# Kernel optimization log

Measured on AMD Instinct MI355X. Metric: run time of the kernel, lower is better.

The kernel has to match this reference:

```python
import jax, jax.numpy as jnp
import numpy as np

E = 8        # num_experts
TOP_K = 2    # num_experts_per_tok
AUX_COEFF = 0.01


def _grok_ffn(x, g, u, d):
    # down(gelu(gate(x)) * up(x)); torch F.gelu default is exact (erf)
    return (jax.nn.gelu(x @ g.T, approximate=False) * (x @ u.T)) @ d.T


def setup_inputs() -> dict:
    key = jax.random.key(0)
    ks = jax.random.split(key, 8)
    B, T, D, H = 4, 4096, 1024, 2816
    s = 0.02
    return {
        "x": jax.random.normal(ks[0], (B, T, D), dtype=jnp.float32),
        "gate_w": jax.random.normal(ks[1], (E, D), dtype=jnp.float32) * 0.01,
        "wg": jax.random.normal(ks[2], (E, H, D), dtype=jnp.float32) * s,
        "wu": jax.random.normal(ks[3], (E, H, D), dtype=jnp.float32) * s,
        "wd": jax.random.normal(ks[4], (E, D, H), dtype=jnp.float32) * s,
        "sg": jax.random.normal(ks[5], (H, D), dtype=jnp.float32) * s,
        "su": jax.random.normal(ks[6], (H, D), dtype=jnp.float32) * s,
        "sd": jax.random.normal(ks[7], (D, H), dtype=jnp.float32) * s,
    }


def reference(x, gate_w, wg, wu, wd, sg, su, sd):
    B, T, D = x.shape
    xf = x.reshape(B * T, D)  # (N, D)

    # ---- router ----
    logits = (xf @ gate_w.T).astype(jnp.float32)          # (N, E)
    top_v, top_i = jax.lax.top_k(logits, TOP_K)           # (N, K)
    expert_weights = jax.nn.softmax(top_v, axis=-1)       # (N, K)
    gates = jax.nn.softmax(logits, axis=-1)               # (N, E)
    f = jax.nn.one_hot(top_i[:, 0], E, dtype=jnp.float32).mean(axis=0)
    P = gates.mean(axis=0)
    aux_loss = AUX_COEFF * E * (f * P).sum()

    # combine weight per (token, expert): sum_k w[t,k] * [idx[t,k]==e]
    onehot = jax.nn.one_hot(top_i, E, dtype=jnp.float32)  # (N, K, E)
    combine = (expert_weights[..., None] * onehot).sum(axis=1)  # (N, E)

    # ---- expert compute (loop over small fixed expert count) ----
    out = jnp.zeros_like(xf)
    for e in range(E):
        out = out + combine[:, e:e + 1] * _grok_ffn(xf, wg[e], wu[e], wd[e])

    out = out.reshape(B, T, D)
    out = out + _grok_ffn(x, sg, su, sd)  # shared expert
    return out, aux_loss
```

## Files before the change

### kernel.cpp

```cpp
#include <hip/hip_runtime.h>
#include <cstdint>

#define NE 8
#define NEX 9
#define NTOK 16384
#define DDIM 1024
#define HDIM 2816

typedef unsigned short u16;
typedef __attribute__((ext_vector_type(8))) short short8;
typedef __attribute__((ext_vector_type(4))) float f32x4;

__device__ __forceinline__ u16 f2bf(float f) {
  uint32_t u = __builtin_bit_cast(uint32_t, f);
  u += 0x7FFFu + ((u >> 16) & 1u);
  return (u16)(u >> 16);
}

__device__ __forceinline__ float wave_reduce_sum(float v) {
  for (int off = 32; off > 0; off >>= 1) v += __shfl_xor(v, off, 64);
  return v;
}

#define GLOAD16(gsrc, ldst)                                                   \
  __builtin_amdgcn_global_load_lds(                                           \
      (const __attribute__((address_space(1))) unsigned int*)(gsrc),          \
      (__attribute__((address_space(3))) unsigned int*)(ldst), 16, 0, 0)

__device__ __forceinline__ void xcd_map(int NT, int MT, int* nt, int* mt) {
  int lin = blockIdx.y * NT + blockIdx.x;
  int nwg = NT * MT;
  int q = nwg >> 3, r = nwg & 7;
  int xcd = lin & 7, idx = lin >> 3;
  int nl = (xcd < r) ? (xcd * (q + 1) + idx) : (r * (q + 1) + (xcd - r) * q + idx);
  *nt = nl / MT;
  *mt = nl % MT;
}

__global__ void init_kernel(int* cnt, float* Pacc, float* fcnt) {
  int t = threadIdx.x;
  if (t < NEX) cnt[t] = (t == 8) ? NTOK : 0;
  if (t < NE) { Pacc[t] = 0.f; fcnt[t] = 0.f; }
}

struct CvtArgs {
  const float* src[7];
  u16* dst[7];
  long long cum[8];
};

__global__ void convert_kernel(CvtArgs a) {
  long long stride = (long long)gridDim.x * blockDim.x;
  long long total = a.cum[7];
  for (long long g = (long long)blockIdx.x * blockDim.x + threadIdx.x; g < total; g += stride) {
    int s = 0;
    while (g >= a.cum[s + 1]) s++;
    long long off = (g - a.cum[s]) * 4;
    float4 v = *reinterpret_cast<const float4*>(a.src[s] + off);
    union { u16 u[4]; uint2 w; } o;
    o.u[0] = f2bf(v.x); o.u[1] = f2bf(v.y); o.u[2] = f2bf(v.z); o.u[3] = f2bf(v.w);
    *reinterpret_cast<uint2*>(a.dst[s] + off) = o.w;
  }
}

__global__ __launch_bounds__(256) void router_kernel(
    const float* __restrict__ x, const float* __restrict__ gw,
    int* __restrict__ tok, float* __restrict__ wtl,
    int* __restrict__ cnt, float* __restrict__ Pacc, float* __restrict__ fcnt,
    u16* __restrict__ xbf) {
  int lane = threadIdx.x & 63;
  int wv = threadIdx.x >> 6;
  __shared__ float red[4][16];
  float pP[NE], pF[NE];
#pragma unroll
  for (int e = 0; e < NE; e++) { pP[e] = 0.f; pF[e] = 0.f; }
  int t0 = blockIdx.x * 16 + wv * 4;
  for (int ti = 0; ti < 4; ti++) {
    int t = t0 + ti;
    float part[NE];
#pragma unroll
    for (int e = 0; e < NE; e++) part[e] = 0.f;
    const float* xp = x + (size_t)t * DDIM;
#pragma unroll
    for (int j = 0; j < 16; j++) {
      float xv = xp[lane + j * 64];
      xbf[(size_t)t * DDIM + lane + j * 64] = f2bf(xv);
#pragma unroll
      for (int e = 0; e < NE; e++) part[e] += xv * gw[e * DDIM + lane + j * 64];
    }
#pragma unroll
    for (int e = 0; e < NE; e++) part[e] = wave_reduce_sum(part[e]);
    if (lane == 0) {
      float v0 = -1e30f, v1 = -1e30f; int i0 = 0, i1 = 0;
#pragma unroll
      for (int e = 0; e < NE; e++) {
        float v = part[e];
        if (v > v0) { v1 = v0; i1 = i0; v0 = v; i0 = e; }
        else if (v > v1) { v1 = v; i1 = e; }
      }
      float e1 = expf(v1 - v0);
      float w0 = 1.f / (1.f + e1);
      float w1 = e1 * w0;
      float s = 0.f, g[NE];
#pragma unroll
      for (int e = 0; e < NE; e++) { g[e] = expf(part[e] - v0); s += g[e]; }
      float inv = 1.f / s;
#pragma unroll
      for (int e = 0; e < NE; e++) pP[e] += g[e] * inv;
      pF[i0] += 1.f;
      int p0 = atomicAdd(&cnt[i0], 1);
      tok[i0 * NTOK + p0] = t; wtl[i0 * NTOK + p0] = w0;
      int p1 = atomicAdd(&cnt[i1], 1);
      tok[i1 * NTOK + p1] = t; wtl[i1 * NTOK + p1] = w1;
      tok[8 * NTOK + t] = t; wtl[8 * NTOK + t] = 1.f;
    }
  }
  if (lane == 0) {
#pragma unroll
    for (int e = 0; e < NE; e++) { red[wv][e] = pP[e]; red[wv][e + 8] = pF[e]; }
  }
  __syncthreads();
  if (threadIdx.x < 16) {
    float s = red[0][threadIdx.x] + red[1][threadIdx.x] + red[2][threadIdx.x] + red[3][threadIdx.x];
    if (threadIdx.x < 8) atomicAdd(&Pacc[threadIdx.x], s);
    else atomicAdd(&fcnt[threadIdx.x - 8], s);
  }
}

__global__ void finalize_router(const int* cnt, int* offs, const float* Pacc,
                                const float* fcnt, float* out_aux) {
  if (threadIdx.x == 0 && blockIdx.x == 0) {
    int p = NTOK;
    for (int e = 0; e < NE; e++) { offs[e] = p; p += cnt[e]; }
    offs[8] = 0;
    float aux = 0.f;
    for (int e = 0; e < NE; e++)
      aux += (fcnt[e] * (1.f / NTOK)) * (Pacc[e] * (1.f / NTOK));
    *out_aux = 0.01f * 8.f * aux;
  }
}


template<bool WB>
__global__ __launch_bounds__(256, 2) void pass1_kernel(
    const u16* __restrict__ xbf, const void* __restrict__ WGall,
    const void* __restrict__ WUall, const void* __restrict__ SG,
    const void* __restrict__ SU, const int* __restrict__ tok,
    const int* __restrict__ cnt, const int* __restrict__ offs,
    u16* __restrict__ Abuf, int e0, int ab_off) {
  int nt, mt;
  xcd_map(gridDim.x, gridDim.y, &nt, &mt);
  int e = e0 + blockIdx.z;
  int Me = cnt[e];
  if (mt * 128 >= Me) return;
  int base = offs[e];
  int ab = (ab_off < 0) ? base : ab_off;

  __shared__ u16 lX[128 * 64];
  __shared__ u16 lG[128 * 64];
  __shared__ u16 lU[128 * 64];

  int tid = threadIdx.x, lane = tid & 63, wv = tid >> 6;
  int wr = wv >> 1, wc = wv & 1;
  size_t wst = (size_t)HDIM * DDIM;
  int swsrc = ((lane & 7) ^ (lane >> 3)) * 8;

  const u16* gx[4];
#pragma unroll
  for (int q = 0; q < 4; q++) {
    int r = (wv * 4 + q) * 8 + (lane >> 3);
    int gm = mt * 128 + r;
    int tk = (gm < Me) ? tok[e * NTOK + gm] : 0;
    gx[q] = xbf + (size_t)tk * DDIM + swsrc;
  }

  const u16 *gg[4], *gu[4];
  const float *pg0 = nullptr, *pu0 = nullptr;
  int st_r0 = 0, st_chunk = 0, st_win = 0;
  if constexpr (WB) {
    const u16* G = (e == 8) ? (const u16*)SG : (const u16*)WGall + (size_t)e * wst;
    const u16* U = (e == 8) ? (const u16*)SU : (const u16*)WUall + (size_t)e * wst;
#pragma unroll
    for (int q = 0; q < 4; q++) {
      int r = (wv * 4 + q) * 8 + (lane >> 3);
      gg[q] = G + (size_t)(nt * 128 + r) * DDIM + swsrc;
      gu[q] = U + (size_t)(nt * 128 + r) * DDIM + swsrc;
    }
  } else {
    const float* G = (e == 8) ? (const float*)SG : (const float*)WGall + (size_t)e * wst;
    const float* U = (e == 8) ? (const float*)SU : (const float*)WUall + (size_t)e * wst;
    st_r0 = wv * 32 + (lane >> 4);
    int c0 = (lane & 15) * 4;
    st_chunk = c0 >> 3; st_win = c0 & 7;
    pg0 = G + (size_t)(nt * 128 + st_r0) * DDIM + c0;
    pu0 = U + (size_t)(nt * 128 + st_r0) * DDIM + c0;
  }

  f32x4 accG[4][4] = {};
  f32x4 accU[4][4] = {};

  for (int kt = 0; kt < DDIM / 64; kt++) {
    __syncthreads();
    int ko = kt * 64;
#pragma unroll
    for (int q = 0; q < 4; q++)
      GLOAD16(gx[q] + ko, lX + (wv * 4 + q) * 512);
    if constexpr (WB) {
#pragma unroll
      for (int q = 0; q < 4; q++) {
        int ldsoff = (wv * 4 + q) * 512;
        GLOAD16(gg[q] + ko, lG + ldsoff);
        GLOAD16(gu[q] + ko, lU + ldsoff);
      }
    } else {
#pragma unroll
      for (int q = 0; q < 8; q++) {
        int row = st_r0 + q * 4;
        int pc = (((st_chunk ^ (row & 7)) << 3) | st_win);
        float4 vg = *reinterpret_cast<const float4*>(pg0 + ko + q * 4 * DDIM);
        float4 vu = *reinterpret_cast<const float4*>(pu0 + ko + q * 4 * DDIM);
        union { u16 h[4]; uint2 w; } og, ou;
        og.h[0] = f2bf(vg.x); og.h[1] = f2bf(vg.y); og.h[2] = f2bf(vg.z); og.h[3] = f2bf(vg.w);
        ou.h[0] = f2bf(vu.x); ou.h[1] = f2bf(vu.y); ou.h[2] = f2bf(vu.z); ou.h[3] = f2bf(vu.w);
        *reinterpret_cast<uint2*>(lG + row * 64 + pc) = og.w;
        *reinterpret_cast<uint2*>(lU + row * 64 + pc) = ou.w;
      }
    }
    asm volatile("s_waitcnt vmcnt(0)" ::: "memory");
    __syncthreads();

    __builtin_amdgcn_s_setprio(1);
#pragma unroll
    for (int kk = 0; kk < 2; kk++) {
      int kbs = (((kk * 4 + (lane >> 4)) ^ (lane & 7))) * 8;
      short8 af[4];
#pragma unroll
      for (int m = 0; m < 4; m++) {
        int row = wr * 64 + m * 16 + (lane & 15);
        af[m] = *reinterpret_cast<const short8*>(lX + row * 64 + kbs);
      }
#pragma unroll
      for (int n = 0; n < 4; n++) {
        int hr = wc * 64 + n * 16 + (lane & 15);
        short8 bg = *reinterpret_cast<const short8*>(lG + hr * 64 + kbs);
        short8 bu = *reinterpret_cast<const short8*>(lU + hr * 64 + kbs);
#pragma unroll
        for (int m = 0; m < 4; m++) {
          accG[m][n] = __builtin_amdgcn_mfma_f32_16x16x32_bf16(af[m], bg, accG[m][n], 0, 0, 0);
          accU[m][n] = __builtin_amdgcn_mfma_f32_16x16x32_bf16(af[m], bu, accU[m][n], 0, 0, 0);
        }
      }
    }
    __builtin_amdgcn_s_setprio(0);
  }

  int rsub = (lane >> 4) * 4, csub = lane & 15;
#pragma unroll
  for (int m = 0; m < 4; m++) {
#pragma unroll
    for (int i = 0; i < 4; i++) {
      int row = wr * 64 + m * 16 + rsub + i;
      int gm = mt * 128 + row;
      if (gm < Me) {
        size_t rb = (size_t)(base + gm - ab) * HDIM + nt * 128;
#pragma unroll
        for (int n = 0; n < 4; n++) {
          float hg = accG[m][n][i];
          float hu = accU[m][n][i];
          float a = 0.5f * hg * (1.f + erff(hg * 0.70710678118f)) * hu;
          Abuf[rb + wc * 64 + n * 16 + csub] = f2bf(a);
        }
      }
    }
  }
}

template<bool WB>
__global__ __launch_bounds__(256, 2) void pass2_kernel(
    const u16* __restrict__ Abuf, const void* __restrict__ WDall,
    const void* __restrict__ SD, const int* __restrict__ tok,
    const float* __restrict__ wtl, const int* __restrict__ cnt,
    const int* __restrict__ offs, float* __restrict__ out, int e0, int ab_off) {
  int nt, mt;
  xcd_map(gridDim.x, gridDim.y, &nt, &mt);
  int e = e0 + blockIdx.z;
  int Me = cnt[e];
  if (mt * 128 >= Me) return;
  int base = offs[e];
  int ab = (ab_off < 0) ? base : ab_off;
  size_t wst = (size_t)HDIM * DDIM;

  __shared__ u16 lA[128 * 64];
  __shared__ u16 lB[128 * 64];

  int tid = threadIdx.x, lane = tid & 63, wv = tid >> 6;
  int wr = wv >> 1, wc = wv & 1;
  int swsrc = ((lane & 7) ^ (lane >> 3)) * 8;

  const u16* ga[4];
#pragma unroll
  for (int q = 0; q < 4; q++) {
    int r = (wv * 4 + q) * 8 + (lane >> 3);
    int slot = base + mt * 128 + r - ab;
    ga[q] = Abuf + (size_t)slot * HDIM + swsrc;
  }

  const u16* gb[4];
  const float* pd0 = nullptr;
  int st_r0 = 0, st_chunk = 0, st_win = 0;
  if constexpr (WB) {
    const u16* D = (e == 8) ? (const u16*)SD : (const u16*)WDall + (size_t)e * wst;
#pragma unroll
    for (int q = 0; q < 4; q++) {
      int r = (wv * 4 + q) * 8 + (lane >> 3);
      gb[q] = D + (size_t)(nt * 128 + r) * HDIM + swsrc;
    }
  } else {
    const float* D = (e == 8) ? (const float*)SD : (const float*)WDall + (size_t)e * wst;
    st_r0 = wv * 32 + (lane >> 4);
    int c0 = (lane & 15) * 4;
    st_chunk = c0 >> 3; st_win = c0 & 7;
    pd0 = D + (size_t)(nt * 128 + st_r0) * HDIM + c0;
  }

  f32x4 acc[4][4] = {};

  for (int kt = 0; kt < HDIM / 64; kt++) {
    __syncthreads();
    int ko = kt * 64;
#pragma unroll
    for (int q = 0; q < 4; q++)
      GLOAD16(ga[q] + ko, lA + (wv * 4 + q) * 512);
    if constexpr (WB) {
#pragma unroll
      for (int q = 0; q < 4; q++)
        GLOAD16(gb[q] + ko, lB + (wv * 4 + q) * 512);
    } else {
#pragma unroll
      for (int q = 0; q < 8; q++) {
        int row = st_r0 + q * 4;
        int pc = (((st_chunk ^ (row & 7)) << 3) | st_win);
        float4 vd = *reinterpret_cast<const float4*>(pd0 + ko + q * 4 * HDIM);
        union { u16 h[4]; uint2 w; } od;
        od.h[0] = f2bf(vd.x); od.h[1] = f2bf(vd.y); od.h[2] = f2bf(vd.z); od.h[3] = f2bf(vd.w);
        *reinterpret_cast<uint2*>(lB + row * 64 + pc) = od.w;
      }
    }
    asm volatile("s_waitcnt vmcnt(0)" ::: "memory");
    __syncthreads();

    __builtin_amdgcn_s_setprio(1);
#pragma unroll
    for (int kk = 0; kk < 2; kk++) {
      int kbs = (((kk * 4 + (lane >> 4)) ^ (lane & 7))) * 8;
      short8 af[4];
#pragma unroll
      for (int m = 0; m < 4; m++) {
        int row = wr * 64 + m * 16 + (lane & 15);
        af[m] = *reinterpret_cast<const short8*>(lA + row * 64 + kbs);
      }
#pragma unroll
      for (int n = 0; n < 4; n++) {
        int dr = wc * 64 + n * 16 + (lane & 15);
        short8 bd = *reinterpret_cast<const short8*>(lB + dr * 64 + kbs);
#pragma unroll
        for (int m = 0; m < 4; m++)
          acc[m][n] = __builtin_amdgcn_mfma_f32_16x16x32_bf16(af[m], bd, acc[m][n], 0, 0, 0);
      }
    }
    __builtin_amdgcn_s_setprio(0);
  }

  int rsub = (lane >> 4) * 4, csub = lane & 15;
#pragma unroll
  for (int m = 0; m < 4; m++) {
#pragma unroll
    for (int i = 0; i < 4; i++) {
      int row = wr * 64 + m * 16 + rsub + i;
      int gm = mt * 128 + row;
      if (gm < Me) {
        int t = tok[e * NTOK + gm];
        float w = (e == 8) ? 1.f : wtl[e * NTOK + gm];
        size_t ob = (size_t)t * DDIM + nt * 128;
#pragma unroll
        for (int n = 0; n < 4; n++) {
          float v = w * acc[m][n][i];
          int c = wc * 64 + n * 16 + csub;
          if (e == 8) out[ob + c] = out[ob + c] + v;
          else atomicAdd(&out[ob + c], v);
        }
      }
    }
  }
}

extern "C" void kernel_launch(void* const* d_in, const int* in_sizes, int n_in,
                              void* d_out, int out_size, void* d_ws, size_t ws_size,
                              hipStream_t stream) {
  const float* x  = (const float*)d_in[0];
  const float* gw = (const float*)d_in[1];
  const float* wg = (const float*)d_in[2];
  const float* wu = (const float*)d_in[3];
  const float* wd = (const float*)d_in[4];
  const float* sg = (const float*)d_in[5];
  const float* su = (const float*)d_in[6];
  const float* sd = (const float*)d_in[7];
  float* out = (float*)d_out;

  bool tierF = ws_size >= 327000000ULL;
  bool tierE = !tierF && ws_size >= 223000000ULL;

  char* ws = (char*)d_ws;
  size_t o = 0;
  auto alloc = [&](size_t bytes) -> void* {
    void* p = ws + o;
    o = (o + bytes + 255) & ~(size_t)255;
    return p;
  };
  u16* xbf = (u16*)alloc((size_t)NTOK * DDIM * 2);
  u16 *wgbf = nullptr, *wubf = nullptr, *sgbf = nullptr, *subf = nullptr;
  u16 *wdbf = nullptr, *sdbf = nullptr;
  if (tierF) {
    wgbf = (u16*)alloc((size_t)NE * HDIM * DDIM * 2);
    wubf = (u16*)alloc((size_t)NE * HDIM * DDIM * 2);
    sgbf = (u16*)alloc((size_t)HDIM * DDIM * 2);
    subf = (u16*)alloc((size_t)HDIM * DDIM * 2);
    wdbf = wgbf;
    sdbf = wgbf + (size_t)NE * DDIM * HDIM;
  }
  size_t abuf_rows = (tierF || tierE) ? ((size_t)2 * NTOK + 128) : ((size_t)NTOK + 128);
  u16* Abuf = (u16*)alloc(abuf_rows * HDIM * 2);
  int*   tok  = (int*)alloc((size_t)NEX * NTOK * 4);
  float* wtl  = (float*)alloc((size_t)NEX * NTOK * 4);
  int*   cnt  = (int*)alloc(64);
  int*   offs = (int*)alloc(64);
  float* Pacc = (float*)alloc(64);
  float* fcnt = (float*)alloc(64);

  hipMemsetAsync(d_out, 0, (size_t)out_size * 4, stream);
  init_kernel<<<1, 64, 0, stream>>>(cnt, Pacc, fcnt);

  if (tierF) {
    CvtArgs ca;
    long long sizes4[7];
    int nsrc = 0;
    ca.src[nsrc] = wg; ca.dst[nsrc] = wgbf; sizes4[nsrc] = (long long)NE * HDIM * DDIM / 4; nsrc++;
    ca.src[nsrc] = wu; ca.dst[nsrc] = wubf; sizes4[nsrc] = (long long)NE * HDIM * DDIM / 4; nsrc++;
    ca.src[nsrc] = sg; ca.dst[nsrc] = sgbf; sizes4[nsrc] = (long long)HDIM * DDIM / 4; nsrc++;
    ca.src[nsrc] = su; ca.dst[nsrc] = subf; sizes4[nsrc] = (long long)HDIM * DDIM / 4; nsrc++;
    ca.cum[0] = 0;
    for (int i = 0; i < 7; i++)
      ca.cum[i + 1] = ca.cum[i] + (i < nsrc ? sizes4[i] : 0);
    convert_kernel<<<4096, 256, 0, stream>>>(ca);
  }

  router_kernel<<<NTOK / 16, 256, 0, stream>>>(x, gw, tok, wtl, cnt, Pacc, fcnt, xbf);
  finalize_router<<<1, 64, 0, stream>>>(cnt, offs, Pacc, fcnt, out + (out_size - 1));

  if (tierF) {
    pass1_kernel<true><<<dim3(HDIM / 128, NTOK / 128, NE), 256, 0, stream>>>(
        xbf, wgbf, wubf, sgbf, subf, tok, cnt, offs, Abuf, 0, NTOK);
    {
      CvtArgs ca;
      ca.src[0] = wd; ca.dst[0] = wdbf;
      ca.src[1] = sd; ca.dst[1] = sdbf;
      long long s0 = (long long)NE * DDIM * HDIM / 4;
      long long s1 = (long long)DDIM * HDIM / 4;
      ca.cum[0] = 0; ca.cum[1] = s0; ca.cum[2] = s0 + s1;
      for (int i = 3; i <= 7; i++) ca.cum[i] = ca.cum[2];
      convert_kernel<<<4096, 256, 0, stream>>>(ca);
    }
    pass2_kernel<true><<<dim3(DDIM / 128, NTOK / 128, NE), 256, 0, stream>>>(
        Abuf, wdbf, sdbf, tok, wtl, cnt, offs, out, 0, NTOK);
    pass1_kernel<true><<<dim3(HDIM / 128, NTOK / 128, 1), 256, 0, stream>>>(
        xbf, wgbf, wubf, sgbf, subf, tok, cnt, offs, Abuf, 8, 0);
    pass2_kernel<true><<<dim3(DDIM / 128, NTOK / 128, 1), 256, 0, stream>>>(
        Abuf, wdbf, sdbf, tok, wtl, cnt, offs, out, 8, 0);
  } else if (tierE) {
    pass1_kernel<false><<<dim3(HDIM / 128, NTOK / 128, 1), 256, 0, stream>>>(
        xbf, wg, wu, sg, su, tok, cnt, offs, Abuf, 8, 0);
    pass2_kernel<false><<<dim3(DDIM / 128, NTOK / 128, 1), 256, 0, stream>>>(
        Abuf, wd, sd, tok, wtl, cnt, offs, out, 8, 0);
    pass1_kernel<false><<<dim3(HDIM / 128, NTOK / 128, NE), 256, 0, stream>>>(
        xbf, wg, wu, sg, su, tok, cnt, offs, Abuf, 0, NTOK);
    pass2_kernel<false><<<dim3(DDIM / 128, NTOK / 128, NE), 256, 0, stream>>>(
        Abuf, wd, sd, tok, wtl, cnt, offs, out, 0, NTOK);
  } else {
    for (int k = 0; k < NEX; k++) {
      int e = (k == 0) ? 8 : (k - 1);
      pass1_kernel<false><<<dim3(HDIM / 128, NTOK / 128, 1), 256, 0, stream>>>(
          xbf, wg, wu, sg, su, tok, cnt, offs, Abuf, e, -1);
      pass2_kernel<false><<<dim3(DDIM / 128, NTOK / 128, 1), 256, 0, stream>>>(
          Abuf, wd, sd, tok, wtl, cnt, offs, out, e, -1);
    }
  }
}
```

Measured before the change: 1.669 ms.

## Load A-operand fragments directly from global memory instead of staging in LDS

Both GEMM passes now skip staging the activation tile (gathered x rows or the intermediate buffer) through shared memory. Each lane reads its MFMA A fragments straight from global memory, and the gathered row pointers are recomputed to match the fragment layout. This removes one LDS buffer per kernel, which could raise occupancy and cut LDS traffic. In exchange, the A data, which is shared by the two column-waves, is read twice from global/L2 with small strided 16-byte loads. Those loads are issued synchronously inside the MFMA loop rather than prefetched.

Measured after the change: 2.324 ms. 39.3% more time.

```diff
diff --git a/kernel.cpp b/kernel.cpp
--- a/kernel.cpp
+++ b/kernel.cpp
@@ -156,7 +156,6 @@
   int base = offs[e];
   int ab = (ab_off < 0) ? base : ab_off;
 
-  __shared__ u16 lX[128 * 64];
   __shared__ u16 lG[128 * 64];
   __shared__ u16 lU[128 * 64];
 
@@ -165,13 +164,12 @@
   size_t wst = (size_t)HDIM * DDIM;
   int swsrc = ((lane & 7) ^ (lane >> 3)) * 8;
 
-  const u16* gx[4];
-#pragma unroll
-  for (int q = 0; q < 4; q++) {
-    int r = (wv * 4 + q) * 8 + (lane >> 3);
-    int gm = mt * 128 + r;
+  const u16* pa[4];
+#pragma unroll
+  for (int m = 0; m < 4; m++) {
+    int gm = mt * 128 + wr * 64 + m * 16 + (lane & 15);
     int tk = (gm < Me) ? tok[e * NTOK + gm] : 0;
-    gx[q] = xbf + (size_t)tk * DDIM + swsrc;
+    pa[m] = xbf + (size_t)tk * DDIM + (lane >> 4) * 8;
   }
 
   const u16 *gg[4], *gu[4];
@@ -202,9 +200,6 @@
   for (int kt = 0; kt < DDIM / 64; kt++) {
     __syncthreads();
     int ko = kt * 64;
-#pragma unroll
-    for (int q = 0; q < 4; q++)
-      GLOAD16(gx[q] + ko, lX + (wv * 4 + q) * 512);
     if constexpr (WB) {
 #pragma unroll
       for (int q = 0; q < 4; q++) {
@@ -235,10 +230,8 @@
       int kbs = (((kk * 4 + (lane >> 4)) ^ (lane & 7))) * 8;
       short8 af[4];
 #pragma unroll
-      for (int m = 0; m < 4; m++) {
-        int row = wr * 64 + m * 16 + (lane & 15);
-        af[m] = *reinterpret_cast<const short8*>(lX + row * 64 + kbs);
-      }
+      for (int m = 0; m < 4; m++)
+        af[m] = *reinterpret_cast<const short8*>(pa[m] + ko + kk * 32);
 #pragma unroll
       for (int n = 0; n < 4; n++) {
         int hr = wc * 64 + n * 16 + (lane & 15);
@@ -290,19 +283,17 @@
   int ab = (ab_off < 0) ? base : ab_off;
   size_t wst = (size_t)HDIM * DDIM;
 
-  __shared__ u16 lA[128 * 64];
   __shared__ u16 lB[128 * 64];
 
   int tid = threadIdx.x, lane = tid & 63, wv = tid >> 6;
   int wr = wv >> 1, wc = wv & 1;
   int swsrc = ((lane & 7) ^ (lane >> 3)) * 8;
 
-  const u16* ga[4];
-#pragma unroll
-  for (int q = 0; q < 4; q++) {
-    int r = (wv * 4 + q) * 8 + (lane >> 3);
-    int slot = base + mt * 128 + r - ab;
-    ga[q] = Abuf + (size_t)slot * HDIM + swsrc;
+  const u16* pa[4];
+#pragma unroll
+  for (int m = 0; m < 4; m++) {
+    int slot = base + mt * 128 + wr * 64 + m * 16 + (lane & 15) - ab;
+    pa[m] = Abuf + (size_t)slot * HDIM + (lane >> 4) * 8;
   }
 
   const u16* gb[4];
@@ -328,9 +319,6 @@
   for (int kt = 0; kt < HDIM / 64; kt++) {
     __syncthreads();
     int ko = kt * 64;
-#pragma unroll
-    for (int q = 0; q < 4; q++)
-      GLOAD16(ga[q] + ko, lA + (wv * 4 + q) * 512);
     if constexpr (WB) {
 #pragma unroll
       for (int q = 0; q < 4; q++)
@@ -355,10 +343,8 @@
       int kbs = (((kk * 4 + (lane >> 4)) ^ (lane & 7))) * 8;
       short8 af[4];
 #pragma unroll
-      for (int m = 0; m < 4; m++) {
-        int row = wr * 64 + m * 16 + (lane & 15);
-        af[m] = *reinterpret_cast<const short8*>(lA + row * 64 + kbs);
-      }
+      for (int m = 0; m < 4; m++)
+        af[m] = *reinterpret_cast<const short8*>(pa[m] + ko + kk * 32);
 #pragma unroll
       for (int n = 0; n < 4; n++) {
         int dr = wc * 64 + n * 16 + (lane & 15);
```
